# Optimization experiments

Measured on AMD Instinct MI355X. Metric: run time of the kernel, lower is better.

The kernel has to match this reference:

```python
import jax, jax.numpy as jnp
import numpy as np

N = 8192
F_IN = 512
F_OUT = 64
ALPHA = 0.2  # LeakyReLU negative slope
MASK_VAL = -9e15


def setup_inputs() -> dict:
    key = jax.random.key(0)
    k1, k2, k3, k4, k5 = jax.random.split(key, 5)
    x = jax.random.normal(k1, (N, F_IN), dtype=jnp.float32)
    adj = jax.random.randint(k2, (N, N), 0, 2, dtype=jnp.int32)
    # params: W uniform(-stdv, stdv) per reset_parameters, A xavier-ish
    stdv = 1.0 / np.sqrt(F_OUT)
    W = jax.random.uniform(k3, (F_IN, F_OUT), dtype=jnp.float32, minval=-stdv, maxval=stdv)
    bias = jax.random.uniform(k4, (F_OUT,), dtype=jnp.float32, minval=-stdv, maxval=stdv)
    A = jax.random.normal(k5, (2 * F_OUT, 1), dtype=jnp.float32) * 0.1
    return {"x": x, "adj": adj, "W": W, "bias": bias, "A": A}


def reference(x, adj, W, bias, A):
    # Wh: [N, F_OUT]
    Wh = x @ W
    # e_ij = leakyrelu([Wh_i || Wh_j] @ A) == leakyrelu(Wh_i @ a1 + Wh_j @ a2)
    # (mathematically identical to the N x N x 2F concat, without materializing it)
    a1 = A[:F_OUT, 0]  # [F_OUT]
    a2 = A[F_OUT:, 0]  # [F_OUT]
    s1 = Wh @ a1  # [N]
    s2 = Wh @ a2  # [N]
    e = jax.nn.leaky_relu(s1[:, None] + s2[None, :], negative_slope=ALPHA)  # [N, N]
    masked = jnp.where(adj > 0, e, MASK_VAL)
    attention = jax.nn.softmax(masked, axis=1)  # [N, N]
    # dropout p=0.0 -> identity
    out = attention @ Wh + bias  # [N, F_OUT]
    return out
```

## Files before the change

### kernel.cpp

```cpp
#include <hip/hip_runtime.h>

#define NN 8192
#define FIN 512
#define FOUT 64
#define LRELU_ALPHA 0.2f
#define MASK_VALF -9000000000000000.0f

typedef __attribute__((ext_vector_type(4))) float f32x4;
typedef __attribute__((ext_vector_type(4))) int i32x4;
typedef __attribute__((ext_vector_type(8))) __bf16 bf16x8;

__global__ __launch_bounds__(256) void gat_wh(
    const float* __restrict__ x, const float* __restrict__ W,
    const float* __restrict__ A,
    __bf16* __restrict__ WhbT, float* __restrict__ s1, float* __restrict__ s2)
{
    const int gid = blockIdx.x * 256 + threadIdx.x;
    const int row = gid >> 4;
    const int cg  = gid & 15;

    f32x4 acc = {0.f, 0.f, 0.f, 0.f};
    const float* xrow = x + (size_t)row * FIN;
    const float* wcol = W + cg * 4;

    #pragma unroll 2
    for (int k = 0; k < FIN; k += 4) {
        f32x4 xv = *reinterpret_cast<const f32x4*>(xrow + k);
        #pragma unroll
        for (int u = 0; u < 4; ++u) {
            f32x4 wv = *reinterpret_cast<const f32x4*>(wcol + (size_t)(k + u) * FOUT);
            acc += xv[u] * wv;
        }
    }

    f32x4 a1v = *reinterpret_cast<const f32x4*>(A + cg * 4);
    f32x4 a2v = *reinterpret_cast<const f32x4*>(A + FOUT + cg * 4);
    float s1p = acc[0]*a1v[0] + acc[1]*a1v[1] + acc[2]*a1v[2] + acc[3]*a1v[3];
    float s2p = acc[0]*a2v[0] + acc[1]*a2v[1] + acc[2]*a2v[2] + acc[3]*a2v[3];
    #pragma unroll
    for (int off = 1; off < 16; off <<= 1) {
        s1p += __shfl_xor(s1p, off);
        s2p += __shfl_xor(s2p, off);
    }
    if (cg == 0) { s1[row] = s1p; s2[row] = s2p; }

    #pragma unroll
    for (int u = 0; u < 4; ++u)
        WhbT[(size_t)(cg * 4 + u) * NN + row] = (__bf16)acc[u];
}

__global__ __launch_bounds__(256) void gat_attn(
    const int* __restrict__ adj, const __bf16* __restrict__ WhbT,
    const float* __restrict__ s1g, const float* __restrict__ s2g,
    const float* __restrict__ bias, float* __restrict__ out)
{
    __shared__ float s2_lds[NN];
    __shared__ float om[4][16];
    __shared__ float ol[4][16];
    __shared__ float oacc[4][16][FOUT];

    const int tid  = threadIdx.x;
    const int w    = tid >> 6;
    const int lane = tid & 63;
    const int r    = lane & 15;
    const int q    = lane >> 4;
    const int row0 = blockIdx.x * 16;

    for (int i = tid; i < NN / 4; i += 256)
        reinterpret_cast<f32x4*>(s2_lds)[i] = reinterpret_cast<const f32x4*>(s2g)[i];
    __syncthreads();

    const float s1r = s1g[row0 + r];

    float m = -INFINITY;
    float l = 0.0f;
    f32x4 acc0 = {0,0,0,0}, acc1 = {0,0,0,0}, acc2 = {0,0,0,0}, acc3 = {0,0,0,0};

    const int*    adjp = adj + (size_t)(row0 + r) * NN + q * 8;
    const __bf16* wp   = WhbT + q * 8;

    for (int it = 0; it < 64; ++it) {
        const int j0 = (w << 11) + (it << 5);

        i32x4 av0 = *reinterpret_cast<const i32x4*>(adjp + j0);
        i32x4 av1 = *reinterpret_cast<const i32x4*>(adjp + j0 + 4);
        bf16x8 b0 = *reinterpret_cast<const bf16x8*>(wp + (size_t)(0 * 16 + r) * NN + j0);
        bf16x8 b1 = *reinterpret_cast<const bf16x8*>(wp + (size_t)(1 * 16 + r) * NN + j0);
        bf16x8 b2 = *reinterpret_cast<const bf16x8*>(wp + (size_t)(2 * 16 + r) * NN + j0);
        bf16x8 b3 = *reinterpret_cast<const bf16x8*>(wp + (size_t)(3 * 16 + r) * NN + j0);
        f32x4 s2a = *reinterpret_cast<const f32x4*>(s2_lds + j0 + q * 8);
        f32x4 s2b = *reinterpret_cast<const f32x4*>(s2_lds + j0 + q * 8 + 4);

        float ev[8];
        #pragma unroll
        for (int i = 0; i < 4; ++i) {
            float t0 = s1r + s2a[i];
            float e0 = fmaxf(t0, LRELU_ALPHA * t0);
            ev[i] = (av0[i] > 0) ? e0 : MASK_VALF;
            float t1 = s1r + s2b[i];
            float e1 = fmaxf(t1, LRELU_ALPHA * t1);
            ev[i + 4] = (av1[i] > 0) ? e1 : MASK_VALF;
        }

        float tmax = ev[0];
        #pragma unroll
        for (int i = 1; i < 8; ++i) tmax = fmaxf(tmax, ev[i]);
        tmax = fmaxf(tmax, __shfl_xor(tmax, 16));
        tmax = fmaxf(tmax, __shfl_xor(tmax, 32));

        const float mnew  = fmaxf(m, tmax);
        const float alpha = __expf(m - mnew);
        m = mnew;

        float psum = 0.f;
        bf16x8 af;
        #pragma unroll
        for (int i = 0; i < 8; ++i) {
            float p = __expf(ev[i] - mnew);
            psum += p;
            af[i] = (__bf16)p;
        }
        psum += __shfl_xor(psum, 16);
        psum += __shfl_xor(psum, 32);
        l = l * alpha + psum;

        const float ar0 = __shfl(alpha, q * 4 + 0);
        const float ar1 = __shfl(alpha, q * 4 + 1);
        const float ar2 = __shfl(alpha, q * 4 + 2);
        const float ar3 = __shfl(alpha, q * 4 + 3);
        f32x4 av = {ar0, ar1, ar2, ar3};
        acc0 *= av; acc1 *= av; acc2 *= av; acc3 *= av;

        acc0 = __builtin_amdgcn_mfma_f32_16x16x32_bf16(af, b0, acc0, 0, 0, 0);
        acc1 = __builtin_amdgcn_mfma_f32_16x16x32_bf16(af, b1, acc1, 0, 0, 0);
        acc2 = __builtin_amdgcn_mfma_f32_16x16x32_bf16(af, b2, acc2, 0, 0, 0);
        acc3 = __builtin_amdgcn_mfma_f32_16x16x32_bf16(af, b3, acc3, 0, 0, 0);
    }

    if (lane < 16) { om[w][lane] = m; ol[w][lane] = l; }
    #pragma unroll
    for (int reg = 0; reg < 4; ++reg) {
        oacc[w][q * 4 + reg][0 * 16 + r] = acc0[reg];
        oacc[w][q * 4 + reg][1 * 16 + r] = acc1[reg];
        oacc[w][q * 4 + reg][2 * 16 + r] = acc2[reg];
        oacc[w][q * 4 + reg][3 * 16 + r] = acc3[reg];
    }
    __syncthreads();

    for (int o = tid; o < 16 * FOUT; o += 256) {
        const int rr = o >> 6;
        const int f  = o & 63;
        const float M = fmaxf(fmaxf(om[0][rr], om[1][rr]), fmaxf(om[2][rr], om[3][rr]));
        float L = 0.f, O = 0.f;
        #pragma unroll
        for (int w2 = 0; w2 < 4; ++w2) {
            const float sc = __expf(om[w2][rr] - M);
            L += sc * ol[w2][rr];
            O += sc * oacc[w2][rr][f];
        }
        out[(size_t)(row0 + rr) * FOUT + f] = O / L + bias[f];
    }
}

extern "C" void kernel_launch(void* const* d_in, const int* in_sizes, int n_in,
                              void* d_out, int out_size, void* d_ws, size_t ws_size,
                              hipStream_t stream)
{
    const float* x    = (const float*)d_in[0];
    const int*   adj  = (const int*)d_in[1];
    const float* W    = (const float*)d_in[2];
    const float* bias = (const float*)d_in[3];
    const float* A    = (const float*)d_in[4];
    float* out = (float*)d_out;

    char* ws = (char*)d_ws;
    __bf16* WhbT = (__bf16*)ws;
    float*  s1   = (float*)(ws + (size_t)FOUT * NN * sizeof(__bf16));
    float*  s2   = s1 + NN;

    gat_wh<<<dim3(NN * 16 / 256), dim3(256), 0, stream>>>(x, W, A, WhbT, s1, s2);
    gat_attn<<<dim3(NN / 16), dim3(256), 0, stream>>>(adj, WhbT, s1, s2, bias, out);
}
```

Measured before the change: 455.2 us.

## Replace online softmax with static row-max bound and split-K Wh projection

```diff
diff --git a/kernel.cpp b/kernel.cpp
--- a/kernel.cpp
+++ b/kernel.cpp
@@ -4,33 +4,47 @@
 #define FIN 512
 #define FOUT 64
 #define LRELU_ALPHA 0.2f
-#define MASK_VALF -9000000000000000.0f
+#define LOG2E 1.4426950408889634f
 
 typedef __attribute__((ext_vector_type(4))) float f32x4;
 typedef __attribute__((ext_vector_type(4))) int i32x4;
 typedef __attribute__((ext_vector_type(8))) __bf16 bf16x8;
+
+#if __has_builtin(__builtin_amdgcn_exp2f)
+#define EXP2F(x) __builtin_amdgcn_exp2f(x)
+#else
+#define EXP2F(x) exp2f(x)
+#endif
 
 __global__ __launch_bounds__(256) void gat_wh(
     const float* __restrict__ x, const float* __restrict__ W,
     const float* __restrict__ A,
     __bf16* __restrict__ WhbT, float* __restrict__ s1, float* __restrict__ s2)
 {
-    const int gid = blockIdx.x * 256 + threadIdx.x;
-    const int row = gid >> 4;
-    const int cg  = gid & 15;
+    const int gid  = blockIdx.x * 256 + threadIdx.x;
+    const int row  = gid >> 6;
+    const int lane = threadIdx.x & 63;
+    const int cg   = lane & 15;
+    const int kh   = lane >> 4;
 
     f32x4 acc = {0.f, 0.f, 0.f, 0.f};
-    const float* xrow = x + (size_t)row * FIN;
-    const float* wcol = W + cg * 4;
+    const float* xrow = x + (size_t)row * FIN + kh * 128;
+    const float* wcol = W + cg * 4 + (size_t)kh * 128 * FOUT;
 
-    #pragma unroll 2
-    for (int k = 0; k < FIN; k += 4) {
+    #pragma unroll 4
+    for (int k = 0; k < 128; k += 4) {
         f32x4 xv = *reinterpret_cast<const f32x4*>(xrow + k);
         #pragma unroll
         for (int u = 0; u < 4; ++u) {
             f32x4 wv = *reinterpret_cast<const f32x4*>(wcol + (size_t)(k + u) * FOUT);
             acc += xv[u] * wv;
         }
+    }
+
+    #pragma unroll
+    for (int u = 0; u < 4; ++u) {
+        acc[u] += __shfl_xor(acc[u], 16);
+        acc[u] += __shfl_xor(acc[u], 32);
     }
 
     f32x4 a1v = *reinterpret_cast<const f32x4*>(A + cg * 4);
@@ -42,11 +56,13 @@
         s1p += __shfl_xor(s1p, off);
         s2p += __shfl_xor(s2p, off);
     }
-    if (cg == 0) { s1[row] = s1p; s2[row] = s2p; }
+    if (lane == 0) { s1[row] = s1p; s2[row] = s2p; }
 
-    #pragma unroll
-    for (int u = 0; u < 4; ++u)
-        WhbT[(size_t)(cg * 4 + u) * NN + row] = (__bf16)acc[u];
+    if (kh == 0) {
+        #pragma unroll
+        for (int u = 0; u < 4; ++u)
+            WhbT[(size_t)(cg * 4 + u) * NN + row] = (__bf16)acc[u];
+    }
 }
 
 __global__ __launch_bounds__(256) void gat_attn(
@@ -54,8 +70,8 @@
     const float* __restrict__ s1g, const float* __restrict__ s2g,
     const float* __restrict__ bias, float* __restrict__ out)
 {
-    __shared__ float s2_lds[NN];
-    __shared__ float om[4][16];
+    __shared__ float s2l[NN];
+    __shared__ float red[4];
     __shared__ float ol[4][16];
     __shared__ float oacc[4][16][FOUT];
 
@@ -66,78 +82,73 @@
     const int q    = lane >> 4;
     const int row0 = blockIdx.x * 16;
 
-    for (int i = tid; i < NN / 4; i += 256)
-        reinterpret_cast<f32x4*>(s2_lds)[i] = reinterpret_cast<const f32x4*>(s2g)[i];
+    float mx = -3.0e38f;
+    for (int i = tid; i < NN / 4; i += 256) {
+        f32x4 v = reinterpret_cast<const f32x4*>(s2g)[i];
+        v *= LOG2E;
+        reinterpret_cast<f32x4*>(s2l)[i] = v;
+        mx = fmaxf(mx, fmaxf(fmaxf(v[0], v[1]), fmaxf(v[2], v[3])));
+    }
+    #pragma unroll
+    for (int off = 1; off < 64; off <<= 1)
+        mx = fmaxf(mx, __shfl_xor(mx, off));
+    if (lane == 0) red[w] = mx;
     __syncthreads();
+    const float s2maxl = fmaxf(fmaxf(red[0], red[1]), fmaxf(red[2], red[3]));
 
-    const float s1r = s1g[row0 + r];
+    const float s1l = s1g[row0 + r] * LOG2E;
+    const float tM  = s1l + s2maxl;
+    const float Ml  = fmaxf(tM, LRELU_ALPHA * tM);
 
-    float m = -INFINITY;
-    float l = 0.0f;
+    float l = 0.f;
     f32x4 acc0 = {0,0,0,0}, acc1 = {0,0,0,0}, acc2 = {0,0,0,0}, acc3 = {0,0,0,0};
 
     const int*    adjp = adj + (size_t)(row0 + r) * NN + q * 8;
     const __bf16* wp   = WhbT + q * 8;
+    const float*  s2b_ = s2l + q * 8;
 
-    for (int it = 0; it < 64; ++it) {
-        const int j0 = (w << 11) + (it << 5);
+    for (int it = 0; it < 32; ++it) {
+        const int j0 = (w << 11) + (it << 6);
+        #pragma unroll
+        for (int c = 0; c < 2; ++c) {
+            const int jc = j0 + (c << 5);
+            i32x4 av0 = *reinterpret_cast<const i32x4*>(adjp + jc);
+            i32x4 av1 = *reinterpret_cast<const i32x4*>(adjp + jc + 4);
+            bf16x8 b0 = *reinterpret_cast<const bf16x8*>(wp + (size_t)(0 * 16 + r) * NN + jc);
+            bf16x8 b1 = *reinterpret_cast<const bf16x8*>(wp + (size_t)(1 * 16 + r) * NN + jc);
+            bf16x8 b2 = *reinterpret_cast<const bf16x8*>(wp + (size_t)(2 * 16 + r) * NN + jc);
+            bf16x8 b3 = *reinterpret_cast<const bf16x8*>(wp + (size_t)(3 * 16 + r) * NN + jc);
+            f32x4 s2a = *reinterpret_cast<const f32x4*>(s2b_ + jc);
+            f32x4 s2c = *reinterpret_cast<const f32x4*>(s2b_ + jc + 4);
 
-        i32x4 av0 = *reinterpret_cast<const i32x4*>(adjp + j0);
-        i32x4 av1 = *reinterpret_cast<const i32x4*>(adjp + j0 + 4);
-        bf16x8 b0 = *reinterpret_cast<const bf16x8*>(wp + (size_t)(0 * 16 + r) * NN + j0);
-        bf16x8 b1 = *reinterpret_cast<const bf16x8*>(wp + (size_t)(1 * 16 + r) * NN + j0);
-        bf16x8 b2 = *reinterpret_cast<const bf16x8*>(wp + (size_t)(2 * 16 + r) * NN + j0);
-        bf16x8 b3 = *reinterpret_cast<const bf16x8*>(wp + (size_t)(3 * 16 + r) * NN + j0);
-        f32x4 s2a = *reinterpret_cast<const f32x4*>(s2_lds + j0 + q * 8);
-        f32x4 s2b = *reinterpret_cast<const f32x4*>(s2_lds + j0 + q * 8 + 4);
-
-        float ev[8];
-        #pragma unroll
-        for (int i = 0; i < 4; ++i) {
-            float t0 = s1r + s2a[i];
-            float e0 = fmaxf(t0, LRELU_ALPHA * t0);
-            ev[i] = (av0[i] > 0) ? e0 : MASK_VALF;
-            float t1 = s1r + s2b[i];
-            float e1 = fmaxf(t1, LRELU_ALPHA * t1);
-            ev[i + 4] = (av1[i] > 0) ? e1 : MASK_VALF;
+            bf16x8 af;
+            float ps = 0.f;
+            #pragma unroll
+            for (int i = 0; i < 4; ++i) {
+                float t0 = s1l + s2a[i];
+                float g0 = fmaxf(t0, LRELU_ALPHA * t0) - Ml;
+                g0 = (av0[i] > 0) ? g0 : -3.0e38f;
+                float p0 = EXP2F(g0);
+                ps += p0;
+                af[i] = (__bf16)p0;
+                float t1 = s1l + s2c[i];
+                float g1 = fmaxf(t1, LRELU_ALPHA * t1) - Ml;
+                g1 = (av1[i] > 0) ? g1 : -3.0e38f;
+                float p1 = EXP2F(g1);
+                ps += p1;
+                af[i + 4] = (__bf16)p1;
+            }
+            l += ps;
+            acc0 = __builtin_amdgcn_mfma_f32_16x16x32_bf16(af, b0, acc0, 0, 0, 0);
+            acc1 = __builtin_amdgcn_mfma_f32_16x16x32_bf16(af, b1, acc1, 0, 0, 0);
+            acc2 = __builtin_amdgcn_mfma_f32_16x16x32_bf16(af, b2, acc2, 0, 0, 0);
+            acc3 = __builtin_amdgcn_mfma_f32_16x16x32_bf16(af, b3, acc3, 0, 0, 0);
         }
-
-        float tmax = ev[0];
-        #pragma unroll
-        for (int i = 1; i < 8; ++i) tmax = fmaxf(tmax, ev[i]);
-        tmax = fmaxf(tmax, __shfl_xor(tmax, 16));
-        tmax = fmaxf(tmax, __shfl_xor(tmax, 32));
-
-        const float mnew  = fmaxf(m, tmax);
-        const float alpha = __expf(m - mnew);
-        m = mnew;
-
-        float psum = 0.f;
-        bf16x8 af;
-        #pragma unroll
-        for (int i = 0; i < 8; ++i) {
-            float p = __expf(ev[i] - mnew);
-            psum += p;
-            af[i] = (__bf16)p;
-        }
-        psum += __shfl_xor(psum, 16);
-        psum += __shfl_xor(psum, 32);
-        l = l * alpha + psum;
-
-        const float ar0 = __shfl(alpha, q * 4 + 0);
-        const float ar1 = __shfl(alpha, q * 4 + 1);
-        const float ar2 = __shfl(alpha, q * 4 + 2);
-        const float ar3 = __shfl(alpha, q * 4 + 3);
-        f32x4 av = {ar0, ar1, ar2, ar3};
-        acc0 *= av; acc1 *= av; acc2 *= av; acc3 *= av;
-
-        acc0 = __builtin_amdgcn_mfma_f32_16x16x32_bf16(af, b0, acc0, 0, 0, 0);
-        acc1 = __builtin_amdgcn_mfma_f32_16x16x32_bf16(af, b1, acc1, 0, 0, 0);
-        acc2 = __builtin_amdgcn_mfma_f32_16x16x32_bf16(af, b2, acc2, 0, 0, 0);
-        acc3 = __builtin_amdgcn_mfma_f32_16x16x32_bf16(af, b3, acc3, 0, 0, 0);
     }
 
-    if (lane < 16) { om[w][lane] = m; ol[w][lane] = l; }
+    l += __shfl_xor(l, 16);
+    l += __shfl_xor(l, 32);
+    if (lane < 16) ol[w][lane] = l;
     #pragma unroll
     for (int reg = 0; reg < 4; ++reg) {
         oacc[w][q * 4 + reg][0 * 16 + r] = acc0[reg];
@@ -150,14 +161,8 @@
     for (int o = tid; o < 16 * FOUT; o += 256) {
         const int rr = o >> 6;
         const int f  = o & 63;
-        const float M = fmaxf(fmaxf(om[0][rr], om[1][rr]), fmaxf(om[2][rr], om[3][rr]));
-        float L = 0.f, O = 0.f;
-        #pragma unroll
-        for (int w2 = 0; w2 < 4; ++w2) {
-            const float sc = __expf(om[w2][rr] - M);
-            L += sc * ol[w2][rr];
-            O += sc * oacc[w2][rr][f];
-        }
+        const float L = ol[0][rr] + ol[1][rr] + ol[2][rr] + ol[3][rr];
+        const float O = oacc[0][rr][f] + oacc[1][rr][f] + oacc[2][rr][f] + oacc[3][rr][f];
         out[(size_t)(row0 + rr) * FOUT + f] = O / L + bias[f];
     }
 }
@@ -178,6 +183,6 @@
     float*  s1   = (float*)(ws + (size_t)FOUT * NN * sizeof(__bf16));
     float*  s2   = s1 + NN;
 
-    gat_wh<<<dim3(NN * 16 / 256), dim3(256), 0, stream>>>(x, W, A, WhbT, s1, s2);
+    gat_wh<<<dim3(NN / 4), dim3(256), 0, stream>>>(x, W, A, WhbT, s1, s2);
     gat_attn<<<dim3(NN / 16), dim3(256), 0, stream>>>(adj, WhbT, s1, s2, bias, out);
 }
```

New measurement: 436.1 us. -4.2%, faster.
